# Optimization experiments

Hardware: AMD Instinct MI355X
Metric: run time of the kernel (lower is better)

## Reference

```python
import jax, jax.numpy as jnp
import numpy as np
from jax import lax

T, B, F = 512, 256, 258
IN, H = 256, 1024


def setup_inputs() -> dict:
    key = jax.random.key(0)
    ks = jax.random.split(key, 6)

    def lin_w(k, fi, fo):
        return jax.random.normal(k, (fi, fo), jnp.float32) * (1.0 / np.sqrt(fi))

    return {
        "u": jax.random.normal(ks[0], (T, B, F), jnp.float32),
        "a": jnp.float32(0.92),
        "b": jnp.float32(-0.3),
        "W0": lin_w(ks[1], IN, H), "b0": jnp.zeros((H,), jnp.float32),
        "W1": lin_w(ks[2], H, H), "b1": jnp.zeros((H,), jnp.float32),
        "W2": lin_w(ks[3], H, H), "b2": jnp.zeros((H,), jnp.float32),
        "W3": lin_w(ks[4], H, 1), "b3": jnp.zeros((1,), jnp.float32),
    }


def reference(u, a, b, W0, b0, W1, b1, W2, b2, W3, b3):
    Tn, Bn, Fn = u.shape
    # MLP over cols 2: — independent of the recurrent state, so batch all timesteps.
    feats = u[:, :, 2:].reshape(Tn * Bn, Fn - 2)
    h = jax.nn.relu(feats @ W0 + b0)
    h = jax.nn.relu(h @ W1 + b1)
    h = jax.nn.relu(h @ W2 + b2)
    net = (h @ W3 + b3).reshape(Tn, Bn)  # [T, B]

    c1 = u[:, :, 1]  # [T, B], multiplied by b each step
    y0 = u[0, :, 0]  # u_y[0]; also the col-0 value used at j=0

    def step(carry, xs):
        net_j, c1_j = xs
        y = a * carry + b * c1_j + net_j
        return y, y

    _, ys = lax.scan(step, y0, (net, c1))  # ys: [T, B] = u_y[1:]
    return jnp.concatenate([y0[None, :], ys], axis=0)  # [T+1, B]
```

## Files before the change

kernel.cpp:

```cpp
#include <hip/hip_runtime.h>
#include <hip/hip_fp16.h>

typedef _Float16 v8h __attribute__((ext_vector_type(8)));
typedef _Float16 v4h __attribute__((ext_vector_type(4)));
typedef float v4f __attribute__((ext_vector_type(4)));

#define T_DIM 512
#define B_DIM 256
#define F_DIM 258
#define IN_DIM 256
#define H_DIM 1024
#define M_ROWS (T_DIM * B_DIM)

__device__ __forceinline__ void tile_map(int b, int nM, int nN, int& mt, int& nt) {
    if (((nM & 7) == 0) && (nN == 8)) {
        int xcd = b & 7;
        int l = b >> 3;
        int mpx = nM >> 3;
        mt = xcd * mpx + (l >> 3);
        nt = l & 7;
    } else {
        mt = b / nN;
        nt = b - mt * nN;
    }
}


__global__ void prep_u_kernel(const float* __restrict__ u,
                              _Float16* __restrict__ X,
                              float* __restrict__ c1, int n) {
    int i = blockIdx.x * blockDim.x + threadIdx.x;
    int stride = gridDim.x * blockDim.x;
    for (; i < n; i += stride) {
        float v = u[i];
        unsigned r = (unsigned)i / 258u;
        unsigned c = (unsigned)i - r * 258u;
        if (c >= 2u) {
            unsigned k = c - 2u;
            X[((r >> 4) * 32u + (k >> 3)) * 128u + (r & 15u) * 8u + (k & 7u)] =
                (_Float16)v;
        } else if (c == 1u) {
            c1[r] = v;
        }
    }
}

__global__ void wt_frag_kernel(const float* __restrict__ W,
                               _Float16* __restrict__ BF, int K, int N) {
    int idx = blockIdx.x * blockDim.x + threadIdx.x;
    int total = (N >> 6) * (K >> 5) * 4 * 64;
    if (idx >= total) return;
    int l = idx & 63;
    int f = idx >> 6;
    int i = f & 3;
    int gk = f >> 2;
    int KC = K >> 5;
    int g = gk / KC, kc = gk - g * KC;
    int col = g * 64 + i * 16 + (l & 15);
    int krow = kc * 32 + (l >> 4) * 8;
    _Float16 tmp[8];
#pragma unroll
    for (int j = 0; j < 8; ++j) tmp[j] = (_Float16)W[(size_t)(krow + j) * N + col];
    *(v8h*)&BF[(size_t)idx * 8] = *(v8h*)tmp;
}

__global__ void wt_vec_kernel(const float* __restrict__ W,
                              _Float16* __restrict__ Wh, int K) {
    int i = blockIdx.x * blockDim.x + threadIdx.x;
    if (i < K) Wh[i] = (_Float16)W[i];
}

__global__ void zero_kernel(float* __restrict__ p, int n) {
    int i = blockIdx.x * blockDim.x + threadIdx.x;
    if (i < n) p[i] = 0.f;
}

__global__ __launch_bounds__(256, 3)
void gemm_f16(const _Float16* __restrict__ Xb, const _Float16* __restrict__ WF,
              const float* __restrict__ bias, _Float16* __restrict__ Cb,
              int M, int N, int K) {
    const int tid = threadIdx.x;
    const int lane = tid & 63;
    const int wave = tid >> 6;
    const int wm = wave >> 1;
    const int wn = wave & 1;
    const int quad = lane >> 4;
    const int r16 = lane & 15;

    int mt, nt;
    tile_map(blockIdx.x, M >> 7, N >> 7, mt, nt);
    const int m0 = mt * 128;
    const int n0 = nt * 128;

    const int KC8 = K >> 3;
    const int NT = K >> 5;

    const int lo_b = (lane >> 4) * 128 + r16 * 8;
    const _Float16* actp[4];
#pragma unroll
    for (int mi = 0; mi < 4; ++mi)
        actp[mi] = Xb + (size_t)((m0 + wm * 64 + mi * 16) >> 4) * KC8 * 128 + lo_b;

    const _Float16* wp = WF + (size_t)(nt * 2 + wn) * NT * 2048 + lane * 8;

    v4f acc[4][4];
#pragma unroll
    for (int i = 0; i < 4; ++i)
#pragma unroll
        for (int j = 0; j < 4; ++j) acc[i][j] = (v4f)0.f;

    for (int kt = 0; kt < NT; ++kt) {
        v8h bfrag[4], afrag[4];
#pragma unroll
        for (int mi = 0; mi < 4; ++mi)
            bfrag[mi] = *(const v8h*)(actp[mi] + (size_t)kt * 512);
#pragma unroll
        for (int ni = 0; ni < 4; ++ni)
            afrag[ni] = *(const v8h*)(wp + (size_t)kt * 2048 + ni * 512);
#pragma unroll
        for (int ni = 0; ni < 4; ++ni)
#pragma unroll
            for (int mi = 0; mi < 4; ++mi)
                acc[ni][mi] = __builtin_amdgcn_mfma_f32_16x16x32_f16(
                    afrag[ni], bfrag[mi], acc[ni][mi], 0, 0, 0);
    }

    const int nb = n0 + wn * 64;
    v4f bv[4];
#pragma unroll
    for (int ni = 0; ni < 4; ++ni)
        bv[ni] = *(const v4f*)&bias[nb + ni * 16 + quad * 4];

    const int NC8 = N >> 3;
#pragma unroll
    for (int ni = 0; ni < 4; ++ni) {
        const int nblk = ((nb + ni * 16) >> 3) + (quad >> 1);
#pragma unroll
        for (int mi = 0; mi < 4; ++mi) {
            v4h hv;
#pragma unroll
            for (int i = 0; i < 4; ++i)
                hv[i] = (_Float16)fmaxf(acc[ni][mi][i] + bv[ni][i], 0.f);
            const size_t mblk = (size_t)((m0 + wm * 64 + mi * 16) >> 4);
            _Float16* dst = Cb + (mblk * NC8 + nblk) * 128 + r16 * 8 + (quad & 1) * 4;
            *(v4h*)dst = hv;
        }
    }
}

__global__ __launch_bounds__(256, 3)
void gemm_dot(const _Float16* __restrict__ Xb, const _Float16* __restrict__ WF,
              const float* __restrict__ bias, const _Float16* __restrict__ w3,
              float* __restrict__ net, int M, int N, int K) {
    const int tid = threadIdx.x;
    const int lane = tid & 63;
    const int wave = tid >> 6;
    const int wm = wave >> 1;
    const int wn = wave & 1;
    const int quad = lane >> 4;
    const int r16 = lane & 15;

    int mt, nt;
    tile_map(blockIdx.x, M >> 7, N >> 7, mt, nt);
    const int m0 = mt * 128;
    const int n0 = nt * 128;

    const int KC8 = K >> 3;
    const int NT = K >> 5;

    const int lo_b = (lane >> 4) * 128 + r16 * 8;
    const _Float16* actp[4];
#pragma unroll
    for (int mi = 0; mi < 4; ++mi)
        actp[mi] = Xb + (size_t)((m0 + wm * 64 + mi * 16) >> 4) * KC8 * 128 + lo_b;

    const _Float16* wp = WF + (size_t)(nt * 2 + wn) * NT * 2048 + lane * 8;

    v4f acc[4][4];
#pragma unroll
    for (int i = 0; i < 4; ++i)
#pragma unroll
        for (int j = 0; j < 4; ++j) acc[i][j] = (v4f)0.f;

    for (int kt = 0; kt < NT; ++kt) {
        v8h bfrag[4], afrag[4];
#pragma unroll
        for (int mi = 0; mi < 4; ++mi)
            bfrag[mi] = *(const v8h*)(actp[mi] + (size_t)kt * 512);
#pragma unroll
        for (int ni = 0; ni < 4; ++ni)
            afrag[ni] = *(const v8h*)(wp + (size_t)kt * 2048 + ni * 512);
#pragma unroll
        for (int ni = 0; ni < 4; ++ni)
#pragma unroll
            for (int mi = 0; mi < 4; ++mi)
                acc[ni][mi] = __builtin_amdgcn_mfma_f32_16x16x32_f16(
                    afrag[ni], bfrag[mi], acc[ni][mi], 0, 0, 0);
    }

    const int nb = n0 + wn * 64;
    v4f bv[4];
    v4h wv[4];
#pragma unroll
    for (int ni = 0; ni < 4; ++ni) {
        bv[ni] = *(const v4f*)&bias[nb + ni * 16 + quad * 4];
        wv[ni] = *(const v4h*)&w3[nb + ni * 16 + quad * 4];
    }

#pragma unroll
    for (int mi = 0; mi < 4; ++mi) {
        float t = 0.f;
#pragma unroll
        for (int ni = 0; ni < 4; ++ni)
#pragma unroll
            for (int i = 0; i < 4; ++i) {
                float v = fmaxf(acc[ni][mi][i] + bv[ni][i], 0.f);
                t = fmaf(v, (float)wv[ni][i], t);
            }
        t += __shfl_xor(t, 16);
        t += __shfl_xor(t, 32);
        if (quad == 0) {
            int row = m0 + wm * 64 + mi * 16 + r16;
            atomicAdd(&net[row], t);
        }
    }
}

__global__ void scan_kernel(const float* __restrict__ net,
                            const float* __restrict__ c1,
                            const float* __restrict__ u,
                            const float* __restrict__ pa,
                            const float* __restrict__ pb,
                            const float* __restrict__ pb3,
                            float* __restrict__ out) {
    const int bidx = threadIdx.x;
    const float a = pa[0];
    const float b = pb[0];
    const float b3 = pb3[0];
    float y = u[(size_t)bidx * F_DIM];
    out[bidx] = y;
#pragma unroll 8
    for (int t = 0; t < T_DIM; ++t) {
        float z = fmaf(b, c1[t * B_DIM + bidx], net[t * B_DIM + bidx] + b3);
        y = fmaf(a, y, z);
        out[(t + 1) * B_DIM + bidx] = y;
    }
}

extern "C" void kernel_launch(void* const* d_in, const int* in_sizes, int n_in,
                              void* d_out, int out_size, void* d_ws, size_t ws_size,
                              hipStream_t stream) {
    const float* u = (const float*)d_in[0];
    const float* pa = (const float*)d_in[1];
    const float* pb = (const float*)d_in[2];
    const float* W0 = (const float*)d_in[3];
    const float* b0 = (const float*)d_in[4];
    const float* W1 = (const float*)d_in[5];
    const float* b1 = (const float*)d_in[6];
    const float* W2 = (const float*)d_in[7];
    const float* b2 = (const float*)d_in[8];
    const float* W3 = (const float*)d_in[9];
    const float* b3 = (const float*)d_in[10];
    float* out = (float*)d_out;

    char* ws = (char*)d_ws;
    size_t off = 0;
    auto alloc = [&](size_t bytes) -> void* {
        void* p = ws + off;
        off += (bytes + 255) & ~(size_t)255;
        return p;
    };

    float* net = (float*)alloc((size_t)M_ROWS * 4);
    float* c1 = (float*)alloc((size_t)M_ROWS * 4);
    _Float16* W0F = (_Float16*)alloc((size_t)IN_DIM * H_DIM * 2);
    _Float16* W1F = (_Float16*)alloc((size_t)H_DIM * H_DIM * 2);
    _Float16* W2F = (_Float16*)alloc((size_t)H_DIM * H_DIM * 2);
    _Float16* W3h = (_Float16*)alloc((size_t)H_DIM * 2);

    const size_t per_row = 512 + 2048 + 2048;
    size_t avail = (ws_size > off + 65536) ? (ws_size - off - 65536) : 0;
    long Rl = (long)(avail / per_row);
    Rl = (Rl / 1024) * 1024;
    if (Rl < 128) Rl = 128;
    if (Rl > M_ROWS) Rl = M_ROWS;
    const int R = (int)Rl;

    _Float16* Xc = (_Float16*)alloc((size_t)R * IN_DIM * 2);
    _Float16* HAc = (_Float16*)alloc((size_t)R * H_DIM * 2);
    _Float16* HBc = (_Float16*)alloc((size_t)R * H_DIM * 2);

    wt_frag_kernel<<<(IN_DIM / 32) * (H_DIM / 64), 256, 0, stream>>>(W0, W0F,
                                                                     IN_DIM, H_DIM);
    wt_frag_kernel<<<(H_DIM / 32) * (H_DIM / 64), 256, 0, stream>>>(W1, W1F,
                                                                    H_DIM, H_DIM);
    wt_frag_kernel<<<(H_DIM / 32) * (H_DIM / 64), 256, 0, stream>>>(W2, W2F,
                                                                    H_DIM, H_DIM);
    wt_vec_kernel<<<4, 256, 0, stream>>>(W3, W3h, H_DIM);
    zero_kernel<<<M_ROWS / 256, 256, 0, stream>>>(net, M_ROWS);

    for (int r0 = 0; r0 < M_ROWS; r0 += R) {
        int Mc = M_ROWS - r0;
        if (Mc > R) Mc = R;
        int nElem = Mc * F_DIM;
        int pgrid = (nElem + 256 * 8 - 1) / (256 * 8);
        if (pgrid > 2048) pgrid = 2048;
        prep_u_kernel<<<pgrid, 256, 0, stream>>>(u + (size_t)r0 * F_DIM, Xc,
                                                 c1 + r0, nElem);

        dim3 blk(256);
        dim3 grd((Mc / 128) * (H_DIM / 128));
        gemm_f16<<<grd, blk, 0, stream>>>(Xc, W0F, b0, HAc, Mc, H_DIM, IN_DIM);
        gemm_f16<<<grd, blk, 0, stream>>>(HAc, W1F, b1, HBc, Mc, H_DIM, H_DIM);
        gemm_dot<<<grd, blk, 0, stream>>>(HBc, W2F, b2, W3h, net + r0, Mc,
                                          H_DIM, H_DIM);
    }

    scan_kernel<<<1, 256, 0, stream>>>(net, c1, u, pa, pb, b3, out);
}
```

Baseline: 1.127 ms.

## Rewrite MLP GEMMs as 256x256 LDS-staged double-buffered kernel with async global-to-LDS loads

```diff
diff --git a/kernel.cpp b/kernel.cpp
--- a/kernel.cpp
+++ b/kernel.cpp
@@ -13,16 +13,24 @@
 #define M_ROWS (T_DIM * B_DIM)
 
 __device__ __forceinline__ void tile_map(int b, int nM, int nN, int& mt, int& nt) {
-    if (((nM & 7) == 0) && (nN == 8)) {
+    if ((nM & 7) == 0) {
         int xcd = b & 7;
         int l = b >> 3;
         int mpx = nM >> 3;
-        mt = xcd * mpx + (l >> 3);
-        nt = l & 7;
+        int lm = l / nN;
+        mt = xcd * mpx + lm;
+        nt = l - lm * nN;
     } else {
-        mt = b / nN;
-        nt = b - mt * nN;
-    }
+        int lm = b / nN;
+        mt = lm;
+        nt = b - lm * nN;
+    }
+}
+
+__device__ __forceinline__ void gl16(const _Float16* g, _Float16* l) {
+    __builtin_amdgcn_global_load_lds(
+        (const __attribute__((address_space(1))) unsigned int*)g,
+        (__attribute__((address_space(3))) unsigned int*)l, 16, 0, 0);
 }
 
 
@@ -75,54 +83,145 @@
     if (i < n) p[i] = 0.f;
 }
 
-__global__ __launch_bounds__(256, 3)
-void gemm_f16(const _Float16* __restrict__ Xb, const _Float16* __restrict__ WF,
-              const float* __restrict__ bias, _Float16* __restrict__ Cb,
-              int M, int N, int K) {
+template <int MI0>
+__device__ __forceinline__ void mfma_pair(v4f (&acc)[8][4], const v8h (&af)[4][2],
+                                          v8h b00, v8h b01, v8h b10, v8h b11) {
+#pragma unroll
+    for (int ni = 0; ni < 4; ++ni) {
+        acc[MI0][ni] = __builtin_amdgcn_mfma_f32_16x16x32_f16(
+            af[ni][0], b00, acc[MI0][ni], 0, 0, 0);
+        acc[MI0][ni] = __builtin_amdgcn_mfma_f32_16x16x32_f16(
+            af[ni][1], b01, acc[MI0][ni], 0, 0, 0);
+        acc[MI0 + 1][ni] = __builtin_amdgcn_mfma_f32_16x16x32_f16(
+            af[ni][0], b10, acc[MI0 + 1][ni], 0, 0, 0);
+        acc[MI0 + 1][ni] = __builtin_amdgcn_mfma_f32_16x16x32_f16(
+            af[ni][1], b11, acc[MI0 + 1][ni], 0, 0, 0);
+    }
+}
+
+template <int DOT>
+__global__ __launch_bounds__(512, 2)
+void gemm256(const _Float16* __restrict__ Xb, const _Float16* __restrict__ WF,
+             const float* __restrict__ bias, const _Float16* __restrict__ w3,
+             _Float16* __restrict__ Cb, float* __restrict__ net,
+             int M, int N, int K) {
+    extern __shared__ _Float16 lds[];
     const int tid = threadIdx.x;
     const int lane = tid & 63;
     const int wave = tid >> 6;
-    const int wm = wave >> 1;
-    const int wn = wave & 1;
+    const int wm = wave >> 2;
+    const int wn = wave & 3;
     const int quad = lane >> 4;
     const int r16 = lane & 15;
+    const int wm8 = wm * 8;
+    const int lrb = (lane >> 4) * 128 + r16 * 8;
 
     int mt, nt;
-    tile_map(blockIdx.x, M >> 7, N >> 7, mt, nt);
-    const int m0 = mt * 128;
-    const int n0 = nt * 128;
-
+    tile_map(blockIdx.x, M >> 8, N >> 8, mt, nt);
+    const int m0 = mt * 256;
+    const int n0 = nt * 256;
+
+    const int KC = K >> 5;
     const int KC8 = K >> 3;
-    const int NT = K >> 5;
-
-    const int lo_b = (lane >> 4) * 128 + r16 * 8;
-    const _Float16* actp[4];
-#pragma unroll
-    for (int mi = 0; mi < 4; ++mi)
-        actp[mi] = Xb + (size_t)((m0 + wm * 64 + mi * 16) >> 4) * KC8 * 128 + lo_b;
-
-    const _Float16* wp = WF + (size_t)(nt * 2 + wn) * NT * 2048 + lane * 8;
-
-    v4f acc[4][4];
-#pragma unroll
-    for (int i = 0; i < 4; ++i)
+    const int NT = K >> 6;
+    const int m016 = m0 >> 4;
+    const int nt4 = nt * 4;
+
+    auto stageA = [&](int g, int kt, _Float16* pa) {
+        gl16(WF + ((size_t)(nt4 + g) * KC + (size_t)kt * 2) * 2048 + tid * 8,
+             pa + g * 4096 + tid * 8);
+    };
+    auto stageB = [&](int mb, int kt, _Float16* pb) {
+        gl16(Xb + ((size_t)(m016 + mb + (tid >> 7)) * KC8 + (size_t)kt * 8) * 128 +
+                 (tid & 127) * 8,
+             pb + mb * 1024 + tid * 8);
+    };
+
+    v4f acc[8][4];
+#pragma unroll
+    for (int i = 0; i < 8; ++i)
 #pragma unroll
         for (int j = 0; j < 4; ++j) acc[i][j] = (v4f)0.f;
 
+    {
+        _Float16* A0 = lds;
+        _Float16* B0 = lds + 16384;
+        stageB(0, 0, B0); stageB(8, 0, B0);
+        stageA(0, 0, A0); stageA(1, 0, A0); stageA(2, 0, A0); stageA(3, 0, A0);
+        stageB(4, 0, B0); stageB(12, 0, B0);
+        asm volatile("s_waitcnt vmcnt(2)" ::: "memory");
+        __builtin_amdgcn_s_barrier();
+    }
+
+#pragma unroll 2
     for (int kt = 0; kt < NT; ++kt) {
-        v8h bfrag[4], afrag[4];
-#pragma unroll
-        for (int mi = 0; mi < 4; ++mi)
-            bfrag[mi] = *(const v8h*)(actp[mi] + (size_t)kt * 512);
-#pragma unroll
-        for (int ni = 0; ni < 4; ++ni)
-            afrag[ni] = *(const v8h*)(wp + (size_t)kt * 2048 + ni * 512);
-#pragma unroll
-        for (int ni = 0; ni < 4; ++ni)
-#pragma unroll
-            for (int mi = 0; mi < 4; ++mi)
-                acc[ni][mi] = __builtin_amdgcn_mfma_f32_16x16x32_f16(
-                    afrag[ni], bfrag[mi], acc[ni][mi], 0, 0, 0);
+        _Float16* pAc = lds + (kt & 1) * 32768;
+        _Float16* pBc = pAc + 16384;
+        _Float16* pAn = lds + ((kt + 1) & 1) * 32768;
+        _Float16* pBn = pAn + 16384;
+        const bool pre = (kt + 1 < NT);
+        const int kn = kt + 1;
+
+        v8h af[4][2];
+
+        {
+#pragma unroll
+            for (int i = 0; i < 4; ++i) {
+                af[i][0] = *(const v8h*)(pAc + wn * 4096 + i * 512 + lane * 8);
+                af[i][1] = *(const v8h*)(pAc + wn * 4096 + (4 + i) * 512 + lane * 8);
+            }
+            v8h b00 = *(const v8h*)(pBc + (wm8 + 0) * 1024 + lrb);
+            v8h b01 = *(const v8h*)(pBc + (wm8 + 0) * 1024 + 512 + lrb);
+            v8h b10 = *(const v8h*)(pBc + (wm8 + 1) * 1024 + lrb);
+            v8h b11 = *(const v8h*)(pBc + (wm8 + 1) * 1024 + 512 + lrb);
+            if (pre) { stageB(0, kn, pBn); stageB(8, kn, pBn); }
+            __builtin_amdgcn_s_barrier();
+            __builtin_amdgcn_s_setprio(1);
+            mfma_pair<0>(acc, af, b00, b01, b10, b11);
+            __builtin_amdgcn_s_setprio(0);
+            __builtin_amdgcn_s_barrier();
+        }
+        {
+            v8h b00 = *(const v8h*)(pBc + (wm8 + 2) * 1024 + lrb);
+            v8h b01 = *(const v8h*)(pBc + (wm8 + 2) * 1024 + 512 + lrb);
+            v8h b10 = *(const v8h*)(pBc + (wm8 + 3) * 1024 + lrb);
+            v8h b11 = *(const v8h*)(pBc + (wm8 + 3) * 1024 + 512 + lrb);
+            if (pre) { stageA(0, kn, pAn); stageA(1, kn, pAn); }
+            __builtin_amdgcn_s_barrier();
+            __builtin_amdgcn_s_setprio(1);
+            mfma_pair<2>(acc, af, b00, b01, b10, b11);
+            __builtin_amdgcn_s_setprio(0);
+            if (pre)
+                asm volatile("s_waitcnt vmcnt(4)" ::: "memory");
+            else
+                asm volatile("s_waitcnt vmcnt(0)" ::: "memory");
+            __builtin_amdgcn_s_barrier();
+        }
+        {
+            v8h b00 = *(const v8h*)(pBc + (wm8 + 4) * 1024 + lrb);
+            v8h b01 = *(const v8h*)(pBc + (wm8 + 4) * 1024 + 512 + lrb);
+            v8h b10 = *(const v8h*)(pBc + (wm8 + 5) * 1024 + lrb);
+            v8h b11 = *(const v8h*)(pBc + (wm8 + 5) * 1024 + 512 + lrb);
+            if (pre) { stageA(2, kn, pAn); stageA(3, kn, pAn); }
+            __builtin_amdgcn_s_barrier();
+            __builtin_amdgcn_s_setprio(1);
+            mfma_pair<4>(acc, af, b00, b01, b10, b11);
+            __builtin_amdgcn_s_setprio(0);
+            __builtin_amdgcn_s_barrier();
+        }
+        {
+            v8h b00 = *(const v8h*)(pBc + (wm8 + 6) * 1024 + lrb);
+            v8h b01 = *(const v8h*)(pBc + (wm8 + 6) * 1024 + 512 + lrb);
+            v8h b10 = *(const v8h*)(pBc + (wm8 + 7) * 1024 + lrb);
+            v8h b11 = *(const v8h*)(pBc + (wm8 + 7) * 1024 + 512 + lrb);
+            if (pre) { stageB(4, kn, pBn); stageB(12, kn, pBn); }
+            __builtin_amdgcn_s_barrier();
+            __builtin_amdgcn_s_setprio(1);
+            mfma_pair<6>(acc, af, b00, b01, b10, b11);
+            __builtin_amdgcn_s_setprio(0);
+            if (pre) asm volatile("s_waitcnt vmcnt(2)" ::: "memory");
+            __builtin_amdgcn_s_barrier();
+        }
     }
 
     const int nb = n0 + wn * 64;
@@ -131,97 +230,44 @@
     for (int ni = 0; ni < 4; ++ni)
         bv[ni] = *(const v4f*)&bias[nb + ni * 16 + quad * 4];
 
-    const int NC8 = N >> 3;
-#pragma unroll
-    for (int ni = 0; ni < 4; ++ni) {
-        const int nblk = ((nb + ni * 16) >> 3) + (quad >> 1);
-#pragma unroll
-        for (int mi = 0; mi < 4; ++mi) {
-            v4h hv;
-#pragma unroll
-            for (int i = 0; i < 4; ++i)
-                hv[i] = (_Float16)fmaxf(acc[ni][mi][i] + bv[ni][i], 0.f);
-            const size_t mblk = (size_t)((m0 + wm * 64 + mi * 16) >> 4);
-            _Float16* dst = Cb + (mblk * NC8 + nblk) * 128 + r16 * 8 + (quad & 1) * 4;
-            *(v4h*)dst = hv;
-        }
-    }
-}
-
-__global__ __launch_bounds__(256, 3)
-void gemm_dot(const _Float16* __restrict__ Xb, const _Float16* __restrict__ WF,
-              const float* __restrict__ bias, const _Float16* __restrict__ w3,
-              float* __restrict__ net, int M, int N, int K) {
-    const int tid = threadIdx.x;
-    const int lane = tid & 63;
-    const int wave = tid >> 6;
-    const int wm = wave >> 1;
-    const int wn = wave & 1;
-    const int quad = lane >> 4;
-    const int r16 = lane & 15;
-
-    int mt, nt;
-    tile_map(blockIdx.x, M >> 7, N >> 7, mt, nt);
-    const int m0 = mt * 128;
-    const int n0 = nt * 128;
-
-    const int KC8 = K >> 3;
-    const int NT = K >> 5;
-
-    const int lo_b = (lane >> 4) * 128 + r16 * 8;
-    const _Float16* actp[4];
-#pragma unroll
-    for (int mi = 0; mi < 4; ++mi)
-        actp[mi] = Xb + (size_t)((m0 + wm * 64 + mi * 16) >> 4) * KC8 * 128 + lo_b;
-
-    const _Float16* wp = WF + (size_t)(nt * 2 + wn) * NT * 2048 + lane * 8;
-
-    v4f acc[4][4];
-#pragma unroll
-    for (int i = 0; i < 4; ++i)
-#pragma unroll
-        for (int j = 0; j < 4; ++j) acc[i][j] = (v4f)0.f;
-
-    for (int kt = 0; kt < NT; ++kt) {
-        v8h bfrag[4], afrag[4];
-#pragma unroll
-        for (int mi = 0; mi < 4; ++mi)
-            bfrag[mi] = *(const v8h*)(actp[mi] + (size_t)kt * 512);
+    if constexpr (DOT == 0) {
+        const int NC8 = N >> 3;
+#pragma unroll
+        for (int ni = 0; ni < 4; ++ni) {
+            const int nblk = ((nb + ni * 16) >> 3) + (quad >> 1);
+#pragma unroll
+            for (int mi = 0; mi < 8; ++mi) {
+                v4h hv;
+#pragma unroll
+                for (int i = 0; i < 4; ++i)
+                    hv[i] = (_Float16)fmaxf(acc[mi][ni][i] + bv[ni][i], 0.f);
+                const size_t mblk = (size_t)((m0 + wm * 128 + mi * 16) >> 4);
+                _Float16* dst =
+                    Cb + (mblk * NC8 + nblk) * 128 + r16 * 8 + (quad & 1) * 4;
+                *(v4h*)dst = hv;
+            }
+        }
+    } else {
+        v4h wv[4];
 #pragma unroll
         for (int ni = 0; ni < 4; ++ni)
-            afrag[ni] = *(const v8h*)(wp + (size_t)kt * 2048 + ni * 512);
-#pragma unroll
-        for (int ni = 0; ni < 4; ++ni)
-#pragma unroll
-            for (int mi = 0; mi < 4; ++mi)
-                acc[ni][mi] = __builtin_amdgcn_mfma_f32_16x16x32_f16(
-                    afrag[ni], bfrag[mi], acc[ni][mi], 0, 0, 0);
-    }
-
-    const int nb = n0 + wn * 64;
-    v4f bv[4];
-    v4h wv[4];
-#pragma unroll
-    for (int ni = 0; ni < 4; ++ni) {
-        bv[ni] = *(const v4f*)&bias[nb + ni * 16 + quad * 4];
-        wv[ni] = *(const v4h*)&w3[nb + ni * 16 + quad * 4];
-    }
-
-#pragma unroll
-    for (int mi = 0; mi < 4; ++mi) {
-        float t = 0.f;
-#pragma unroll
-        for (int ni = 0; ni < 4; ++ni)
-#pragma unroll
-            for (int i = 0; i < 4; ++i) {
-                float v = fmaxf(acc[ni][mi][i] + bv[ni][i], 0.f);
-                t = fmaf(v, (float)wv[ni][i], t);
+            wv[ni] = *(const v4h*)&w3[nb + ni * 16 + quad * 4];
+#pragma unroll
+        for (int mi = 0; mi < 8; ++mi) {
+            float t = 0.f;
+#pragma unroll
+            for (int ni = 0; ni < 4; ++ni)
+#pragma unroll
+                for (int i = 0; i < 4; ++i) {
+                    float v = fmaxf(acc[mi][ni][i] + bv[ni][i], 0.f);
+                    t = fmaf(v, (float)wv[ni][i], t);
+                }
+            t += __shfl_xor(t, 16);
+            t += __shfl_xor(t, 32);
+            if (quad == 0) {
+                int row = m0 + wm * 128 + mi * 16 + r16;
+                atomicAdd(&net[row], t);
             }
-        t += __shfl_xor(t, 16);
-        t += __shfl_xor(t, 32);
-        if (quad == 0) {
-            int row = m0 + wm * 64 + mi * 16 + r16;
-            atomicAdd(&net[row], t);
         }
     }
 }
@@ -281,8 +327,8 @@
     const size_t per_row = 512 + 2048 + 2048;
     size_t avail = (ws_size > off + 65536) ? (ws_size - off - 65536) : 0;
     long Rl = (long)(avail / per_row);
-    Rl = (Rl / 1024) * 1024;
-    if (Rl < 128) Rl = 128;
+    Rl = (Rl / 2048) * 2048;
+    if (Rl < 2048) Rl = 2048;
     if (Rl > M_ROWS) Rl = M_ROWS;
     const int R = (int)Rl;
 
@@ -299,6 +345,7 @@
     wt_vec_kernel<<<4, 256, 0, stream>>>(W3, W3h, H_DIM);
     zero_kernel<<<M_ROWS / 256, 256, 0, stream>>>(net, M_ROWS);
 
+    const size_t lds_bytes = 131072;
     for (int r0 = 0; r0 < M_ROWS; r0 += R) {
         int Mc = M_ROWS - r0;
         if (Mc > R) Mc = R;
@@ -308,12 +355,14 @@
         prep_u_kernel<<<pgrid, 256, 0, stream>>>(u + (size_t)r0 * F_DIM, Xc,
                                                  c1 + r0, nElem);
 
-        dim3 blk(256);
-        dim3 grd((Mc / 128) * (H_DIM / 128));
-        gemm_f16<<<grd, blk, 0, stream>>>(Xc, W0F, b0, HAc, Mc, H_DIM, IN_DIM);
-        gemm_f16<<<grd, blk, 0, stream>>>(HAc, W1F, b1, HBc, Mc, H_DIM, H_DIM);
-        gemm_dot<<<grd, blk, 0, stream>>>(HBc, W2F, b2, W3h, net + r0, Mc,
-                                          H_DIM, H_DIM);
+        dim3 blk(512);
+        dim3 grd((Mc / 256) * (H_DIM / 256));
+        gemm256<0><<<grd, blk, lds_bytes, stream>>>(Xc, W0F, b0, nullptr, HAc,
+                                                    nullptr, Mc, H_DIM, IN_DIM);
+        gemm256<0><<<grd, blk, lds_bytes, stream>>>(HAc, W1F, b1, nullptr, HBc,
+                                                    nullptr, Mc, H_DIM, H_DIM);
+        gemm256<1><<<grd, blk, lds_bytes, stream>>>(HBc, W2F, b2, W3h, nullptr,
+                                                    net + r0, Mc, H_DIM, H_DIM);
     }
 
     scan_kernel<<<1, 256, 0, stream>>>(net, c1, u, pa, pb, b3, out);
```

Result: faster. 946.3 us (-16.1%).
